# Performance work log

Hardware: AMD Instinct MI355X
Metric: run time of the kernel (lower is better)

The kernel has to match this reference:

```python
import jax, jax.numpy as jnp
import numpy as np

EPS = 0.5          # residual scaling (module __init__ eps)
N = 100_000        # num nodes
E = 1_250_000      # num edges (avg degree ~12.5)
D = 64             # feature dim


def setup_inputs() -> dict:
    key = jax.random.key(0)
    k1, k2, k3 = jax.random.split(key, 3)
    x = jax.random.normal(k1, (N, D), dtype=jnp.float32)
    src = jax.random.randint(k2, (E,), 0, N, dtype=jnp.int32)
    dst = jax.random.randint(k3, (E,), 0, N, dtype=jnp.int32)
    return {"x": x, "src": src, "dst": dst}


def reference(x, src, dst):
    n = x.shape[0]
    # out-degree of each node = number of edges with that node as source
    deg = jax.ops.segment_sum(jnp.ones(src.shape, dtype=x.dtype), src, num_segments=n)
    norm = jnp.power(jnp.maximum(deg, 1.0), -0.5)          # [N]
    edge_norm = norm[src] * norm[dst]                      # [E] (u_mul_v)
    msg = x[src] * edge_norm[:, None]                      # [E, D] (u_mul_e)
    h = jax.ops.segment_sum(msg, dst, num_segments=n)      # sum per destination
    return h + x * EPS
```

## Files before the change

### kernel.cpp

```cpp
#include <hip/hip_runtime.h>

constexpr int D        = 64;
constexpr float EPS    = 0.5f;
constexpr int BKT      = 256;
constexpr int CAPB_MAX = 4096;
constexpr int EPB      = 8192;
constexpr int PTHREADS = 512;
constexpr int EPT      = EPB / PTHREADS;
constexpr int GTHREADS = 1024;
constexpr int NBMAX    = 1024;
constexpr int MAXOVF   = 65536;

__device__ __forceinline__ unsigned int f2bf(float f) {
    unsigned int u = __float_as_uint(f);
    return (u + 0x7FFFu + ((u >> 16) & 1u)) >> 16;
}
__device__ __forceinline__ float bf2f_lo(unsigned int v) { return __uint_as_float(v << 16); }
__device__ __forceinline__ float bf2f_hi(unsigned int v) { return __uint_as_float(v & 0xFFFF0000u); }


__global__ __launch_bounds__(PTHREADS)
void partition_kernel(const int* __restrict__ src, const int* __restrict__ dst,
                      int* __restrict__ curD, int* __restrict__ curS,
                      unsigned int* __restrict__ rec, unsigned char* __restrict__ srec,
                      int* __restrict__ ovf_cnt, int* __restrict__ ovf,
                      int* __restrict__ sovf_cnt, int* __restrict__ sovf,
                      int E, int NB, int capb) {
    __shared__ int histD[NBMAX];
    __shared__ int histS[NBMAX];
    __shared__ int startD[NBMAX];
    __shared__ int startS[NBMAX];
    const int base = blockIdx.x * EPB;
    const int tid  = threadIdx.x;
    const bool full = (base + EPB) <= E;
    for (int b = tid; b < NB; b += PTHREADS) { histD[b] = 0; histS[b] = 0; }
    __syncthreads();

    if (full) {
        const int4* s4 = (const int4*)(src + base);
        const int4* d4 = (const int4*)(dst + base);
        #pragma unroll
        for (int k = 0; k < EPT / 4; ++k) {
            int4 sv = s4[tid + k * PTHREADS];
            int4 dv = d4[tid + k * PTHREADS];
            atomicAdd(&histD[dv.x >> 8], 1); atomicAdd(&histS[sv.x >> 8], 1);
            atomicAdd(&histD[dv.y >> 8], 1); atomicAdd(&histS[sv.y >> 8], 1);
            atomicAdd(&histD[dv.z >> 8], 1); atomicAdd(&histS[sv.z >> 8], 1);
            atomicAdd(&histD[dv.w >> 8], 1); atomicAdd(&histS[sv.w >> 8], 1);
        }
    } else {
        for (int k = 0; k < EPT; ++k) {
            int e = base + tid + k * PTHREADS;
            if (e < E) {
                atomicAdd(&histD[dst[e] >> 8], 1);
                atomicAdd(&histS[src[e] >> 8], 1);
            }
        }
    }
    __syncthreads();
    for (int b = tid; b < NB; b += PTHREADS) {
        int c = histD[b];
        startD[b] = (c > 0) ? atomicAdd(&curD[b], c) : 0;
        histD[b] = 0;
        int c2 = histS[b];
        startS[b] = (c2 > 0) ? atomicAdd(&curS[b], c2) : 0;
        histS[b] = 0;
    }
    __syncthreads();
    if (full) {
        const int4* s4 = (const int4*)(src + base);
        const int4* d4 = (const int4*)(dst + base);
        #pragma unroll
        for (int k = 0; k < EPT / 4; ++k) {
            int4 sv = s4[tid + k * PTHREADS];
            int4 dv = d4[tid + k * PTHREADS];
            int ss[4] = {sv.x, sv.y, sv.z, sv.w};
            int tt[4] = {dv.x, dv.y, dv.z, dv.w};
            #pragma unroll
            for (int j = 0; j < 4; ++j) {
                int s = ss[j], t = tt[j];
                int bD = t >> 8;
                int r  = atomicAdd(&histD[bD], 1);
                int p  = startD[bD] + r;
                if (p < capb) {
                    rec[(size_t)bD * capb + p] = ((unsigned int)s << 8) | (unsigned int)(t & (BKT - 1));
                } else {
                    int i = atomicAdd(ovf_cnt, 1);
                    if (i < MAXOVF) { ovf[2 * i] = s; ovf[2 * i + 1] = t; }
                }
                int bS = s >> 8;
                int r2 = atomicAdd(&histS[bS], 1);
                int p2 = startS[bS] + r2;
                if (p2 < capb) {
                    srec[(size_t)bS * capb + p2] = (unsigned char)(s & (BKT - 1));
                } else {
                    int i = atomicAdd(sovf_cnt, 1);
                    if (i < MAXOVF) sovf[i] = s;
                }
            }
        }
    } else {
        for (int k = 0; k < EPT; ++k) {
            int e = base + tid + k * PTHREADS;
            if (e < E) {
                int s = src[e], t = dst[e];
                int bD = t >> 8;
                int r  = atomicAdd(&histD[bD], 1);
                int p  = startD[bD] + r;
                if (p < capb) {
                    rec[(size_t)bD * capb + p] = ((unsigned int)s << 8) | (unsigned int)(t & (BKT - 1));
                } else {
                    int i = atomicAdd(ovf_cnt, 1);
                    if (i < MAXOVF) { ovf[2 * i] = s; ovf[2 * i + 1] = t; }
                }
                int bS = s >> 8;
                int r2 = atomicAdd(&histS[bS], 1);
                int p2 = startS[bS] + r2;
                if (p2 < capb) {
                    srec[(size_t)bS * capb + p2] = (unsigned char)(s & (BKT - 1));
                } else {
                    int i = atomicAdd(sovf_cnt, 1);
                    if (i < MAXOVF) sovf[i] = s;
                }
            }
        }
    }
}

__global__ __launch_bounds__(256)
void normyh_kernel(const unsigned char* __restrict__ srec, const int* __restrict__ curS,
                   const int* __restrict__ sovf_cnt, const int* __restrict__ sovf,
                   const float2* __restrict__ x2, unsigned int* __restrict__ yh,
                   float* __restrict__ norm, int n, int capb) {
    const int b   = blockIdx.x;
    const int tid = threadIdx.x;
    __shared__ int hist[BKT];
    __shared__ float nrm[BKT];
    hist[tid] = 0;
    __syncthreads();
    int cnt = curS[b];
    if (cnt > capb) cnt = capb;
    const unsigned int* s4 = (const unsigned int*)(srec + (size_t)b * capb);
    int nw = cnt >> 2;
    for (int i = tid; i < nw; i += 256) {
        unsigned int w = s4[i];
        atomicAdd(&hist[w & 255u], 1);
        atomicAdd(&hist[(w >> 8) & 255u], 1);
        atomicAdd(&hist[(w >> 16) & 255u], 1);
        atomicAdd(&hist[w >> 24], 1);
    }
    for (int i = (nw << 2) + tid; i < cnt; i += 256)
        atomicAdd(&hist[srec[(size_t)b * capb + i]], 1);
    int oc = *sovf_cnt;
    if (oc > 0) {
        if (oc > MAXOVF) oc = MAXOVF;
        for (int i = tid; i < oc; i += 256) {
            int s = sovf[i];
            if ((s >> 8) == b) atomicAdd(&hist[s & (BKT - 1)], 1);
        }
    }
    __syncthreads();
    int node = b * BKT + tid;
    float nm = rsqrtf(fmaxf((float)hist[tid], 1.0f));
    nrm[tid] = nm;
    if (node < n) norm[node] = nm;
    __syncthreads();
    int nodes = n - b * BKT;
    if (nodes > BKT) nodes = BKT;
    if (nodes < 0) nodes = 0;
    int total = nodes * (D / 2);
    size_t gbase = (size_t)b * BKT * (D / 2);
    for (int i = tid; i < total; i += 256) {
        float2 v = x2[gbase + i];
        float nm2 = nrm[i >> 5];
        yh[gbase + i] = f2bf(v.x * nm2) | (f2bf(v.y * nm2) << 16);
    }
}

__global__ __launch_bounds__(GTHREADS)
void sortgather_kernel(const unsigned int* __restrict__ rec, const int* __restrict__ curD,
                       const float* __restrict__ norm, const uint4* __restrict__ yr4,
                       const float4* __restrict__ x4, float4* __restrict__ out4,
                       int n, int capb) {
    __shared__ unsigned int recs[CAPB_MAX];
    __shared__ int srcs[CAPB_MAX];
    __shared__ int hist[BKT];
    __shared__ int rankb[BKT];
    __shared__ int rsL[BKT];
    __shared__ float nrmL[BKT];
    __shared__ int wsum[BKT / 64];
    const int b   = blockIdx.x;
    const int tid = threadIdx.x;

    int cnt = curD[b];
    if (cnt > capb) cnt = capb;
    for (int i = tid; i < cnt; i += GTHREADS) recs[i] = rec[(size_t)b * capb + i];
    if (tid < BKT) {
        hist[tid] = 0;
        int node = b * BKT + tid;
        nrmL[tid] = (node < n) ? norm[node] : 1.0f;
    }
    __syncthreads();
    for (int i = tid; i < cnt; i += GTHREADS) atomicAdd(&hist[recs[i] & (BKT - 1)], 1);
    __syncthreads();
    {
        const int lane = tid & 63;
        int v = (tid < BKT) ? hist[tid] : 0;
        #pragma unroll
        for (int off = 1; off < 64; off <<= 1) {
            int t = __shfl_up(v, off);
            if (lane >= off) v += t;
        }
        if (tid < BKT && lane == 63) wsum[tid >> 6] = v;
        __syncthreads();
        if (tid < BKT) {
            int w = tid >> 6, add = 0;
            #pragma unroll
            for (int i = 0; i < BKT / 64; ++i)
                if (i < w) add += wsum[i];
            int excl = v + add - hist[tid];
            rankb[tid] = excl;
            rsL[tid]   = excl;
        }
    }
    __syncthreads();
    for (int i = tid; i < cnt; i += GTHREADS) {
        unsigned int v = recs[i];
        int pos = atomicAdd(&rankb[v & (BKT - 1)], 1);
        srcs[pos] = (int)(v >> 8);
    }
    __syncthreads();

    const int wave = tid >> 6;
    const int lane = tid & 63;
    const int fl   = lane & 7;
    const int oct  = lane >> 3;
    #pragma unroll
    for (int r = 0; r < BKT / 128; ++r) {
        int ln   = r * 128 + wave * 8 + oct;
        int node = b * BKT + ln;
        bool valid = node < n;
        int rsl = valid ? rsL[ln]  : 0;
        int cl  = valid ? hist[ln] : 0;
        int m = cl;
        m = max(m, __shfl_xor(m, 8));
        m = max(m, __shfl_xor(m, 16));
        m = max(m, __shfl_xor(m, 32));
        float a0 = 0.f, a1 = 0.f, a2 = 0.f, a3 = 0.f;
        float a4 = 0.f, a5 = 0.f, a6 = 0.f, a7 = 0.f;
        for (int k = 0; k < m; k += 8) {
            int sb[8];
            #pragma unroll
            for (int j = 0; j < 8; ++j) {
                int kj = k + j;
                sb[j] = (kj < cl) ? srcs[rsl + kj] : -1;
            }
            #pragma unroll
            for (int j = 0; j < 8; ++j) {
                bool take = sb[j] >= 0;
                int s = take ? sb[j] : 0;
                uint4 v = yr4[(size_t)s * 8 + fl];
                if (!take) { v.x = 0u; v.y = 0u; v.z = 0u; v.w = 0u; }
                a0 += bf2f_lo(v.x); a1 += bf2f_hi(v.x);
                a2 += bf2f_lo(v.y); a3 += bf2f_hi(v.y);
                a4 += bf2f_lo(v.z); a5 += bf2f_hi(v.z);
                a6 += bf2f_lo(v.w); a7 += bf2f_hi(v.w);
            }
        }
        if (valid) {
            float nt = nrmL[ln];
            size_t basei = (size_t)node * 16 + fl * 2;
            float4 xv0 = x4[basei], xv1 = x4[basei + 1];
            float4 r0, r1;
            r0.x = a0 * nt + EPS * xv0.x;  r0.y = a1 * nt + EPS * xv0.y;
            r0.z = a2 * nt + EPS * xv0.z;  r0.w = a3 * nt + EPS * xv0.w;
            r1.x = a4 * nt + EPS * xv1.x;  r1.y = a5 * nt + EPS * xv1.y;
            r1.z = a6 * nt + EPS * xv1.z;  r1.w = a7 * nt + EPS * xv1.w;
            out4[basei] = r0;
            out4[basei + 1] = r1;
        }
    }
}

__global__ void cleanup_kernel(const float* __restrict__ x, const float* __restrict__ norm,
                               const int* __restrict__ ovf_cnt, const int* __restrict__ ovf,
                               float* __restrict__ out) {
    int cnt = *ovf_cnt;
    if (cnt > MAXOVF) cnt = MAXOVF;
    long long total = (long long)cnt * D;
    long long stride = (long long)gridDim.x * blockDim.x;
    for (long long i = blockIdx.x * (long long)blockDim.x + threadIdx.x; i < total; i += stride) {
        int e = (int)(i >> 6), d = (int)(i & 63);
        int s = ovf[2 * e], t = ovf[2 * e + 1];
        atomicAdd(&out[(size_t)t * D + d], norm[s] * norm[t] * x[(size_t)s * D + d]);
    }
}


__global__ void fb_hist(const int* __restrict__ src, int* __restrict__ deg, int E) {
    int e = blockIdx.x * blockDim.x + threadIdx.x;
    if (e < E) atomicAdd(&deg[src[e]], 1);
}
__global__ void fb_norm(const int* __restrict__ deg, float* __restrict__ norm, int n) {
    int i = blockIdx.x * blockDim.x + threadIdx.x;
    if (i < n) norm[i] = rsqrtf(fmaxf((float)deg[i], 1.0f));
}
__global__ void fb_init_out(const float4* __restrict__ x, float4* __restrict__ out, int n4) {
    int i = blockIdx.x * blockDim.x + threadIdx.x;
    if (i < n4) {
        float4 v = x[i];
        out[i] = make_float4(v.x * EPS, v.y * EPS, v.z * EPS, v.w * EPS);
    }
}
__global__ void fb_scatter(const float* __restrict__ x, const int* __restrict__ src,
                           const int* __restrict__ dst, const float* __restrict__ norm,
                           float* __restrict__ out, int E) {
    long long tid = (long long)blockIdx.x * blockDim.x + threadIdx.x;
    int e = (int)(tid >> 6), d = (int)(tid & 63);
    if (e < E) {
        int s = src[e], t = dst[e];
        atomicAdd(&out[(size_t)t * D + d], norm[s] * norm[t] * x[(size_t)s * D + d]);
    }
}


extern "C" void kernel_launch(void* const* d_in, const int* in_sizes, int n_in,
                              void* d_out, int out_size, void* d_ws, size_t ws_size,
                              hipStream_t stream) {
    const float* x   = (const float*)d_in[0];
    const int*   src = (const int*)d_in[1];
    const int*   dst = (const int*)d_in[2];
    float* out = (float*)d_out;

    const int ND = in_sizes[0];
    const int E  = in_sizes[1];
    const int n  = ND / D;
    const int NB = (n + BKT - 1) / BKT;
    constexpr int B = 256;
    const int NB64 = (NB + 63) & ~63;

    int capb = 0;
    for (int c : {4096, 3584}) {
        size_t srecB = ((size_t)NB * c + 15) & ~15ull;
        size_t need = (size_t)NB * c * 4
                    + srecB
                    + (size_t)ND * 2
                    + (size_t)n * 4
                    + (size_t)(2 * NB64 + 128) * 4
                    + (size_t)3 * MAXOVF * 4;
        if (need <= ws_size) { capb = c; break; }
    }

    if (NB <= NBMAX && capb > 0 && n < (1 << 24)) {
        unsigned int* rec   = (unsigned int*)d_ws;
        unsigned char* srec = (unsigned char*)(rec + (size_t)NB * capb);
        size_t srecB        = ((size_t)NB * capb + 15) & ~15ull;
        unsigned int* yh    = (unsigned int*)(srec + srecB);
        float* norm         = (float*)(yh + ND / 2);
        int* curD           = (int*)(norm + n);
        int* curS           = curD + NB64;
        int* ovf_cnt        = curS + NB64;
        int* sovf_cnt       = ovf_cnt + 64;
        int* ovf            = sovf_cnt + 64;
        int* sovf           = ovf + 2 * MAXOVF;

        hipMemsetAsync(curD, 0, (size_t)(2 * NB64 + 128) * 4, stream);
        partition_kernel<<<(E + EPB - 1) / EPB, PTHREADS, 0, stream>>>(src, dst, curD, curS,
                                                                       rec, srec, ovf_cnt, ovf,
                                                                       sovf_cnt, sovf, E, NB, capb);
        normyh_kernel<<<NB, B, 0, stream>>>(srec, curS, sovf_cnt, sovf,
                                            (const float2*)x, yh, norm, n, capb);
        sortgather_kernel<<<NB, GTHREADS, 0, stream>>>(rec, curD, norm, (const uint4*)yh,
                                                       (const float4*)x, (float4*)out, n, capb);
        cleanup_kernel<<<32, B, 0, stream>>>(x, norm, ovf_cnt, ovf, out);
    } else {
        int*   deg  = (int*)d_ws;
        float* norm = (float*)d_ws + n;
        hipMemsetAsync(deg, 0, (size_t)n * sizeof(int), stream);
        fb_hist<<<(E + B - 1) / B, B, 0, stream>>>(src, deg, E);
        fb_norm<<<(n + B - 1) / B, B, 0, stream>>>(deg, norm, n);
        fb_init_out<<<(ND / 4 + B - 1) / B, B, 0, stream>>>((const float4*)x, (float4*)out, ND / 4);
        long long total = (long long)E * D;
        fb_scatter<<<(int)((total + B - 1) / B), B, 0, stream>>>(x, src, dst, norm, out, E);
    }
}
```

Measured before the change: 140.7 us.

## Replace global atomic bucketing with per-block local sort and offset tables

The partition kernel now counting-sorts its edge chunk in shared memory and writes the sorted chunk contiguously. It also records per-block bucket offset tables, replacing global atomic cursors, fixed-capacity buckets, overflow lists, the memset and the cleanup kernel. The norm and gather kernels rebuild each bucket by scanning the offset tables and pulling the small per-block segments. The gather kernel processes oversized buckets in chunks. This removes global atomics and scattered global writes, but adds many short, poorly coalesced segment reads and strided table reads downstream.

```diff
diff --git a/kernel.cpp b/kernel.cpp
--- a/kernel.cpp
+++ b/kernel.cpp
@@ -3,13 +3,13 @@
 constexpr int D        = 64;
 constexpr float EPS    = 0.5f;
 constexpr int BKT      = 256;
-constexpr int CAPB_MAX = 4096;
-constexpr int EPB      = 8192;
+constexpr int CAPB     = 6144;
+constexpr int EPB      = 4096;
 constexpr int PTHREADS = 512;
 constexpr int EPT      = EPB / PTHREADS;
 constexpr int GTHREADS = 1024;
 constexpr int NBMAX    = 1024;
-constexpr int MAXOVF   = 65536;
+constexpr int MAXBLK   = 1024;
 
 __device__ __forceinline__ unsigned int f2bf(float f) {
     unsigned int u = __float_as_uint(f);
@@ -21,18 +21,26 @@
 
 __global__ __launch_bounds__(PTHREADS)
 void partition_kernel(const int* __restrict__ src, const int* __restrict__ dst,
-                      int* __restrict__ curD, int* __restrict__ curS,
-                      unsigned int* __restrict__ rec, unsigned char* __restrict__ srec,
-                      int* __restrict__ ovf_cnt, int* __restrict__ ovf,
-                      int* __restrict__ sovf_cnt, int* __restrict__ sovf,
-                      int E, int NB, int capb) {
+                      unsigned int* __restrict__ recB, unsigned char* __restrict__ srecB,
+                      unsigned short* __restrict__ tabD, unsigned short* __restrict__ tabS,
+                      int E, int NB, int NBP) {
+    __shared__ unsigned int  srt[EPB];
+    __shared__ unsigned char ssrt[EPB];
     __shared__ int histD[NBMAX];
     __shared__ int histS[NBMAX];
-    __shared__ int startD[NBMAX];
-    __shared__ int startS[NBMAX];
-    const int base = blockIdx.x * EPB;
+    __shared__ unsigned int rsD[NBMAX];
+    __shared__ unsigned int rsS[NBMAX];
+    __shared__ unsigned int wsums[PTHREADS / 64];
+    __shared__ unsigned int carry;
+
+    const int blk  = blockIdx.x;
+    const int base = blk * EPB;
     const int tid  = threadIdx.x;
-    const bool full = (base + EPB) <= E;
+    const int lane = tid & 63;
+    const int wid  = tid >> 6;
+    const int cnt  = min(EPB, E - base);
+    const bool full = (cnt == EPB);
+
     for (int b = tid; b < NB; b += PTHREADS) { histD[b] = 0; histS[b] = 0; }
     __syncthreads();
 
@@ -50,23 +58,73 @@
         }
     } else {
         for (int k = 0; k < EPT; ++k) {
-            int e = base + tid + k * PTHREADS;
-            if (e < E) {
-                atomicAdd(&histD[dst[e] >> 8], 1);
-                atomicAdd(&histS[src[e] >> 8], 1);
-            }
-        }
-    }
-    __syncthreads();
-    for (int b = tid; b < NB; b += PTHREADS) {
-        int c = histD[b];
-        startD[b] = (c > 0) ? atomicAdd(&curD[b], c) : 0;
-        histD[b] = 0;
-        int c2 = histS[b];
-        startS[b] = (c2 > 0) ? atomicAdd(&curS[b], c2) : 0;
-        histS[b] = 0;
-    }
-    __syncthreads();
+            int e = tid + k * PTHREADS;
+            if (e < cnt) {
+                atomicAdd(&histD[dst[base + e] >> 8], 1);
+                atomicAdd(&histS[src[base + e] >> 8], 1);
+            }
+        }
+    }
+    __syncthreads();
+
+    if (tid == 0) carry = 0;
+    __syncthreads();
+    for (int bp = 0; bp < NB; bp += PTHREADS) {
+        int idx = bp + tid;
+        unsigned int orig = (idx < NB) ? (unsigned int)histD[idx] : 0u;
+        if (idx < NB) histD[idx] = 0;
+        unsigned int v = orig;
+        #pragma unroll
+        for (int off = 1; off < 64; off <<= 1) {
+            unsigned int t = __shfl_up(v, off);
+            if (lane >= off) v += t;
+        }
+        if (lane == 63) wsums[wid] = v;
+        __syncthreads();
+        unsigned int add = carry;
+        for (int w = 0; w < wid; ++w) add += wsums[w];
+        if (idx < NB) rsD[idx] = v - orig + add;
+        __syncthreads();
+        if (tid == 0) {
+            unsigned int s = carry;
+            for (int w = 0; w < PTHREADS / 64; ++w) s += wsums[w];
+            carry = s;
+        }
+        __syncthreads();
+    }
+    if (tid == 0) carry = 0;
+    __syncthreads();
+    for (int bp = 0; bp < NB; bp += PTHREADS) {
+        int idx = bp + tid;
+        unsigned int orig = (idx < NB) ? (unsigned int)histS[idx] : 0u;
+        if (idx < NB) histS[idx] = 0;
+        unsigned int v = orig;
+        #pragma unroll
+        for (int off = 1; off < 64; off <<= 1) {
+            unsigned int t = __shfl_up(v, off);
+            if (lane >= off) v += t;
+        }
+        if (lane == 63) wsums[wid] = v;
+        __syncthreads();
+        unsigned int add = carry;
+        for (int w = 0; w < wid; ++w) add += wsums[w];
+        if (idx < NB) rsS[idx] = v - orig + add;
+        __syncthreads();
+        if (tid == 0) {
+            unsigned int s = carry;
+            for (int w = 0; w < PTHREADS / 64; ++w) s += wsums[w];
+            carry = s;
+        }
+        __syncthreads();
+    }
+
+    for (int b = tid; b <= NB; b += PTHREADS) {
+        unsigned short vD = (unsigned short)((b < NB) ? rsD[b] : (unsigned int)cnt);
+        unsigned short vS = (unsigned short)((b < NB) ? rsS[b] : (unsigned int)cnt);
+        tabD[(size_t)blk * NBP + b] = vD;
+        tabS[(size_t)blk * NBP + b] = vS;
+    }
+
     if (full) {
         const int4* s4 = (const int4*)(src + base);
         const int4* d4 = (const int4*)(dst + base);
@@ -81,83 +139,53 @@
                 int s = ss[j], t = tt[j];
                 int bD = t >> 8;
                 int r  = atomicAdd(&histD[bD], 1);
-                int p  = startD[bD] + r;
-                if (p < capb) {
-                    rec[(size_t)bD * capb + p] = ((unsigned int)s << 8) | (unsigned int)(t & (BKT - 1));
-                } else {
-                    int i = atomicAdd(ovf_cnt, 1);
-                    if (i < MAXOVF) { ovf[2 * i] = s; ovf[2 * i + 1] = t; }
-                }
+                srt[rsD[bD] + r] = ((unsigned int)s << 8) | (unsigned int)(t & (BKT - 1));
                 int bS = s >> 8;
                 int r2 = atomicAdd(&histS[bS], 1);
-                int p2 = startS[bS] + r2;
-                if (p2 < capb) {
-                    srec[(size_t)bS * capb + p2] = (unsigned char)(s & (BKT - 1));
-                } else {
-                    int i = atomicAdd(sovf_cnt, 1);
-                    if (i < MAXOVF) sovf[i] = s;
-                }
+                ssrt[rsS[bS] + r2] = (unsigned char)(s & (BKT - 1));
             }
         }
     } else {
         for (int k = 0; k < EPT; ++k) {
-            int e = base + tid + k * PTHREADS;
-            if (e < E) {
-                int s = src[e], t = dst[e];
+            int e = tid + k * PTHREADS;
+            if (e < cnt) {
+                int s = src[base + e], t = dst[base + e];
                 int bD = t >> 8;
                 int r  = atomicAdd(&histD[bD], 1);
-                int p  = startD[bD] + r;
-                if (p < capb) {
-                    rec[(size_t)bD * capb + p] = ((unsigned int)s << 8) | (unsigned int)(t & (BKT - 1));
-                } else {
-                    int i = atomicAdd(ovf_cnt, 1);
-                    if (i < MAXOVF) { ovf[2 * i] = s; ovf[2 * i + 1] = t; }
-                }
+                srt[rsD[bD] + r] = ((unsigned int)s << 8) | (unsigned int)(t & (BKT - 1));
                 int bS = s >> 8;
                 int r2 = atomicAdd(&histS[bS], 1);
-                int p2 = startS[bS] + r2;
-                if (p2 < capb) {
-                    srec[(size_t)bS * capb + p2] = (unsigned char)(s & (BKT - 1));
-                } else {
-                    int i = atomicAdd(sovf_cnt, 1);
-                    if (i < MAXOVF) sovf[i] = s;
-                }
-            }
-        }
+                ssrt[rsS[bS] + r2] = (unsigned char)(s & (BKT - 1));
+            }
+        }
+    }
+    __syncthreads();
+
+    {
+        uint4* go = (uint4*)(recB + (size_t)blk * EPB);
+        const uint4* gi = (const uint4*)srt;
+        for (int i = tid; i < EPB / 4; i += PTHREADS) go[i] = gi[i];
+        uint4* so = (uint4*)(srecB + (size_t)blk * EPB);
+        const uint4* si = (const uint4*)ssrt;
+        for (int i = tid; i < EPB / 16; i += PTHREADS) so[i] = si[i];
     }
 }
 
 __global__ __launch_bounds__(256)
-void normyh_kernel(const unsigned char* __restrict__ srec, const int* __restrict__ curS,
-                   const int* __restrict__ sovf_cnt, const int* __restrict__ sovf,
+void normyh_kernel(const unsigned char* __restrict__ srecB, const unsigned short* __restrict__ tabS,
                    const float2* __restrict__ x2, unsigned int* __restrict__ yh,
-                   float* __restrict__ norm, int n, int capb) {
+                   float* __restrict__ norm, int n, int NBLK, int NBP) {
     const int b   = blockIdx.x;
     const int tid = threadIdx.x;
     __shared__ int hist[BKT];
     __shared__ float nrm[BKT];
     hist[tid] = 0;
     __syncthreads();
-    int cnt = curS[b];
-    if (cnt > capb) cnt = capb;
-    const unsigned int* s4 = (const unsigned int*)(srec + (size_t)b * capb);
-    int nw = cnt >> 2;
-    for (int i = tid; i < nw; i += 256) {
-        unsigned int w = s4[i];
-        atomicAdd(&hist[w & 255u], 1);
-        atomicAdd(&hist[(w >> 8) & 255u], 1);
-        atomicAdd(&hist[(w >> 16) & 255u], 1);
-        atomicAdd(&hist[w >> 24], 1);
-    }
-    for (int i = (nw << 2) + tid; i < cnt; i += 256)
-        atomicAdd(&hist[srec[(size_t)b * capb + i]], 1);
-    int oc = *sovf_cnt;
-    if (oc > 0) {
-        if (oc > MAXOVF) oc = MAXOVF;
-        for (int i = tid; i < oc; i += 256) {
-            int s = sovf[i];
-            if ((s >> 8) == b) atomicAdd(&hist[s & (BKT - 1)], 1);
-        }
+    for (int blk = tid; blk < NBLK; blk += 256) {
+        int o0 = tabS[(size_t)blk * NBP + b];
+        int o1 = tabS[(size_t)blk * NBP + b + 1];
+        const unsigned char* p = srecB + (size_t)blk * EPB;
+        for (int j = o0; j < o1; ++j) atomicAdd(&hist[p[j]], 1);
     }
     __syncthreads();
     int node = b * BKT + tid;
@@ -178,121 +206,163 @@
 }
 
 __global__ __launch_bounds__(GTHREADS)
-void sortgather_kernel(const unsigned int* __restrict__ rec, const int* __restrict__ curD,
+void sortgather_kernel(const unsigned int* __restrict__ recB, const unsigned short* __restrict__ tabD,
                        const float* __restrict__ norm, const uint4* __restrict__ yr4,
                        const float4* __restrict__ x4, float4* __restrict__ out4,
-                       int n, int capb) {
-    __shared__ unsigned int recs[CAPB_MAX];
-    __shared__ int srcs[CAPB_MAX];
+                       int n, int NBLK, int NBP) {
+    __shared__ unsigned int recs[CAPB];
+    __shared__ unsigned int srcs[CAPB];
+    __shared__ unsigned short segoff[MAXBLK];
+    __shared__ unsigned int dstoff[MAXBLK + 1];
     __shared__ int hist[BKT];
     __shared__ int rankb[BKT];
     __shared__ int rsL[BKT];
     __shared__ float nrmL[BKT];
-    __shared__ int wsum[BKT / 64];
-    const int b   = blockIdx.x;
-    const int tid = threadIdx.x;
-
-    int cnt = curD[b];
-    if (cnt > capb) cnt = capb;
-    for (int i = tid; i < cnt; i += GTHREADS) recs[i] = rec[(size_t)b * capb + i];
+    __shared__ unsigned int wsums[GTHREADS / 64];
+    __shared__ unsigned int carry;
+    const int b    = blockIdx.x;
+    const int tid  = threadIdx.x;
+    const int lane = tid & 63;
+    const int wid  = tid >> 6;
+
+    for (int blk = tid; blk < NBLK; blk += GTHREADS) {
+        unsigned int o0 = tabD[(size_t)blk * NBP + b];
+        unsigned int o1 = tabD[(size_t)blk * NBP + b + 1];
+        segoff[blk] = (unsigned short)o0;
+        dstoff[blk] = o1 - o0;
+    }
     if (tid < BKT) {
-        hist[tid] = 0;
         int node = b * BKT + tid;
         nrmL[tid] = (node < n) ? norm[node] : 1.0f;
     }
-    __syncthreads();
-    for (int i = tid; i < cnt; i += GTHREADS) atomicAdd(&hist[recs[i] & (BKT - 1)], 1);
-    __syncthreads();
-    {
-        const int lane = tid & 63;
-        int v = (tid < BKT) ? hist[tid] : 0;
+    if (tid == 0) carry = 0;
+    __syncthreads();
+    for (int bp = 0; bp < NBLK; bp += GTHREADS) {
+        int idx = bp + tid;
+        unsigned int orig = (idx < NBLK) ? dstoff[idx] : 0u;
+        unsigned int v = orig;
         #pragma unroll
         for (int off = 1; off < 64; off <<= 1) {
-            int t = __shfl_up(v, off);
+            unsigned int t = __shfl_up(v, off);
             if (lane >= off) v += t;
         }
-        if (tid < BKT && lane == 63) wsum[tid >> 6] = v;
-        __syncthreads();
-        if (tid < BKT) {
-            int w = tid >> 6, add = 0;
+        if (lane == 63) wsums[wid] = v;
+        __syncthreads();
+        unsigned int add = carry;
+        for (int w = 0; w < wid; ++w) add += wsums[w];
+        if (idx < NBLK) dstoff[idx] = v - orig + add;
+        __syncthreads();
+        if (tid == 0) {
+            unsigned int s = carry;
+            for (int w = 0; w < GTHREADS / 64; ++w) s += wsums[w];
+            carry = s;
+        }
+        __syncthreads();
+    }
+    if (tid == 0) dstoff[NBLK] = carry;
+    __syncthreads();
+    const int cnt = (int)dstoff[NBLK];
+    const int nch = (cnt > CAPB) ? (cnt + CAPB - 1) / CAPB : 1;
+
+    const int fl  = lane & 7;
+    const int oct = lane >> 3;
+
+    for (int c = 0; c < nch; ++c) {
+        const unsigned int lo = (unsigned int)c * CAPB;
+        const unsigned int hi = min((unsigned int)cnt, lo + (unsigned int)CAPB);
+        const int wlen = (int)(hi - lo);
+        for (int blk = wid; blk < NBLK; blk += GTHREADS / 64) {
+            unsigned int dbase = dstoff[blk], dend = dstoff[blk + 1];
+            unsigned int s0 = max(dbase, lo), s1 = min(dend, hi);
+            if (s0 < s1) {
+                size_t glo = (size_t)blk * EPB + segoff[blk] + (s0 - dbase);
+                for (unsigned int j = lane; j < s1 - s0; j += 64)
+                    recs[s0 - lo + j] = recB[glo + j];
+            }
+        }
+        __syncthreads();
+        if (tid < BKT) hist[tid] = 0;
+        __syncthreads();
+        for (int i = tid; i < wlen; i += GTHREADS) atomicAdd(&hist[recs[i] & (BKT - 1)], 1);
+        __syncthreads();
+        {
+            int v = (tid < BKT) ? hist[tid] : 0;
             #pragma unroll
-            for (int i = 0; i < BKT / 64; ++i)
-                if (i < w) add += wsum[i];
-            int excl = v + add - hist[tid];
-            rankb[tid] = excl;
-            rsL[tid]   = excl;
-        }
-    }
-    __syncthreads();
-    for (int i = tid; i < cnt; i += GTHREADS) {
-        unsigned int v = recs[i];
-        int pos = atomicAdd(&rankb[v & (BKT - 1)], 1);
-        srcs[pos] = (int)(v >> 8);
-    }
-    __syncthreads();
-
-    const int wave = tid >> 6;
-    const int lane = tid & 63;
-    const int fl   = lane & 7;
-    const int oct  = lane >> 3;
-    #pragma unroll
-    for (int r = 0; r < BKT / 128; ++r) {
-        int ln   = r * 128 + wave * 8 + oct;
-        int node = b * BKT + ln;
-        bool valid = node < n;
-        int rsl = valid ? rsL[ln]  : 0;
-        int cl  = valid ? hist[ln] : 0;
-        int m = cl;
-        m = max(m, __shfl_xor(m, 8));
-        m = max(m, __shfl_xor(m, 16));
-        m = max(m, __shfl_xor(m, 32));
-        float a0 = 0.f, a1 = 0.f, a2 = 0.f, a3 = 0.f;
-        float a4 = 0.f, a5 = 0.f, a6 = 0.f, a7 = 0.f;
-        for (int k = 0; k < m; k += 8) {
-            int sb[8];
-            #pragma unroll
-            for (int j = 0; j < 8; ++j) {
-                int kj = k + j;
-                sb[j] = (kj < cl) ? srcs[rsl + kj] : -1;
-            }
-            #pragma unroll
-            for (int j = 0; j < 8; ++j) {
-                bool take = sb[j] >= 0;
-                int s = take ? sb[j] : 0;
-                uint4 v = yr4[(size_t)s * 8 + fl];
-                if (!take) { v.x = 0u; v.y = 0u; v.z = 0u; v.w = 0u; }
-                a0 += bf2f_lo(v.x); a1 += bf2f_hi(v.x);
-                a2 += bf2f_lo(v.y); a3 += bf2f_hi(v.y);
-                a4 += bf2f_lo(v.z); a5 += bf2f_hi(v.z);
-                a6 += bf2f_lo(v.w); a7 += bf2f_hi(v.w);
-            }
-        }
-        if (valid) {
-            float nt = nrmL[ln];
-            size_t basei = (size_t)node * 16 + fl * 2;
-            float4 xv0 = x4[basei], xv1 = x4[basei + 1];
-            float4 r0, r1;
-            r0.x = a0 * nt + EPS * xv0.x;  r0.y = a1 * nt + EPS * xv0.y;
-            r0.z = a2 * nt + EPS * xv0.z;  r0.w = a3 * nt + EPS * xv0.w;
-            r1.x = a4 * nt + EPS * xv1.x;  r1.y = a5 * nt + EPS * xv1.y;
-            r1.z = a6 * nt + EPS * xv1.z;  r1.w = a7 * nt + EPS * xv1.w;
-            out4[basei] = r0;
-            out4[basei + 1] = r1;
-        }
-    }
-}
-
-__global__ void cleanup_kernel(const float* __restrict__ x, const float* __restrict__ norm,
-                               const int* __restrict__ ovf_cnt, const int* __restrict__ ovf,
-                               float* __restrict__ out) {
-    int cnt = *ovf_cnt;
-    if (cnt > MAXOVF) cnt = MAXOVF;
-    long long total = (long long)cnt * D;
-    long long stride = (long long)gridDim.x * blockDim.x;
-    for (long long i = blockIdx.x * (long long)blockDim.x + threadIdx.x; i < total; i += stride) {
-        int e = (int)(i >> 6), d = (int)(i & 63);
-        int s = ovf[2 * e], t = ovf[2 * e + 1];
-        atomicAdd(&out[(size_t)t * D + d], norm[s] * norm[t] * x[(size_t)s * D + d]);
+            for (int off = 1; off < 64; off <<= 1) {
+                int t = __shfl_up(v, off);
+                if (lane >= off) v += t;
+            }
+            if (tid < BKT && lane == 63) wsums[wid] = (unsigned int)v;
+            __syncthreads();
+            if (tid < BKT) {
+                int add = 0;
+                for (int w = 0; w < wid; ++w) add += (int)wsums[w];
+                int excl = v + add - hist[tid];
+                rankb[tid] = excl;
+                rsL[tid]   = excl;
+            }
+        }
+        __syncthreads();
+        for (int i = tid; i < wlen; i += GTHREADS) {
+            unsigned int v = recs[i];
+            int pos = atomicAdd(&rankb[v & (BKT - 1)], 1);
+            srcs[pos] = (int)(v >> 8);
+        }
+        __syncthreads();
+
+        #pragma unroll
+        for (int r = 0; r < BKT / 128; ++r) {
+            int ln   = r * 128 + wid * 8 + oct;
+            int node = b * BKT + ln;
+            bool valid = node < n;
+            int rsl = valid ? rsL[ln]  : 0;
+            int cl  = valid ? hist[ln] : 0;
+            int m = cl;
+            m = max(m, __shfl_xor(m, 8));
+            m = max(m, __shfl_xor(m, 16));
+            m = max(m, __shfl_xor(m, 32));
+            float a0 = 0.f, a1 = 0.f, a2 = 0.f, a3 = 0.f;
+            float a4 = 0.f, a5 = 0.f, a6 = 0.f, a7 = 0.f;
+            for (int k = 0; k < m; k += 8) {
+                int sb[8];
+                #pragma unroll
+                for (int j = 0; j < 8; ++j) {
+                    int kj = k + j;
+                    sb[j] = (kj < cl) ? (int)srcs[rsl + kj] : -1;
+                }
+                #pragma unroll
+                for (int j = 0; j < 8; ++j) {
+                    bool take = sb[j] >= 0;
+                    int s = take ? sb[j] : 0;
+                    uint4 v = yr4[(size_t)s * 8 + fl];
+                    if (!take) { v.x = 0u; v.y = 0u; v.z = 0u; v.w = 0u; }
+                    a0 += bf2f_lo(v.x); a1 += bf2f_hi(v.x);
+                    a2 += bf2f_lo(v.y); a3 += bf2f_hi(v.y);
+                    a4 += bf2f_lo(v.z); a5 += bf2f_hi(v.z);
+                    a6 += bf2f_lo(v.w); a7 += bf2f_hi(v.w);
+                }
+            }
+            if (valid) {
+                float nt = nrmL[ln];
+                size_t basei = (size_t)node * 16 + fl * 2;
+                float4 r0, r1;
+                if (c == 0) {
+                    float4 xv0 = x4[basei], xv1 = x4[basei + 1];
+                    r0.x = a0 * nt + EPS * xv0.x;  r0.y = a1 * nt + EPS * xv0.y;
+                    r0.z = a2 * nt + EPS * xv0.z;  r0.w = a3 * nt + EPS * xv0.w;
+                    r1.x = a4 * nt + EPS * xv1.x;  r1.y = a5 * nt + EPS * xv1.y;
+                    r1.z = a6 * nt + EPS * xv1.z;  r1.w = a7 * nt + EPS * xv1.w;
+                } else {
+                    float4 p0 = out4[basei], p1 = out4[basei + 1];
+                    r0.x = p0.x + a0 * nt;  r0.y = p0.y + a1 * nt;
+                    r0.z = p0.z + a2 * nt;  r0.w = p0.w + a3 * nt;
+                    r1.x = p1.x + a4 * nt;  r1.y = p1.y + a5 * nt;
+                    r1.z = p1.z + a6 * nt;  r1.w = p1.w + a7 * nt;
+                }
+                out4[basei] = r0;
+                out4[basei + 1] = r1;
+            }
+        }
     }
 }
 
@@ -335,44 +405,37 @@
     const int ND = in_sizes[0];
     const int E  = in_sizes[1];
     const int n  = ND / D;
-    const int NB = (n + BKT - 1) / BKT;
+    const int NB   = (n + BKT - 1) / BKT;
+    const int NBLK = (E + EPB - 1) / EPB;
+    const int NBP  = NB + 1;
     constexpr int B = 256;
-    const int NB64 = (NB + 63) & ~63;
-
-    int capb = 0;
-    for (int c : {4096, 3584}) {
-        size_t srecB = ((size_t)NB * c + 15) & ~15ull;
-        size_t need = (size_t)NB * c * 4
-                    + srecB
-                    + (size_t)ND * 2
-                    + (size_t)n * 4
-                    + (size_t)(2 * NB64 + 128) * 4
-                    + (size_t)3 * MAXOVF * 4;
-        if (need <= ws_size) { capb = c; break; }
-    }
-
-    if (NB <= NBMAX && capb > 0 && n < (1 << 24)) {
-        unsigned int* rec   = (unsigned int*)d_ws;
-        unsigned char* srec = (unsigned char*)(rec + (size_t)NB * capb);
-        size_t srecB        = ((size_t)NB * capb + 15) & ~15ull;
-        unsigned int* yh    = (unsigned int*)(srec + srecB);
-        float* norm         = (float*)(yh + ND / 2);
-        int* curD           = (int*)(norm + n);
-        int* curS           = curD + NB64;
-        int* ovf_cnt        = curS + NB64;
-        int* sovf_cnt       = ovf_cnt + 64;
-        int* ovf            = sovf_cnt + 64;
-        int* sovf           = ovf + 2 * MAXOVF;
-
-        hipMemsetAsync(curD, 0, (size_t)(2 * NB64 + 128) * 4, stream);
-        partition_kernel<<<(E + EPB - 1) / EPB, PTHREADS, 0, stream>>>(src, dst, curD, curS,
-                                                                       rec, srec, ovf_cnt, ovf,
-                                                                       sovf_cnt, sovf, E, NB, capb);
-        normyh_kernel<<<NB, B, 0, stream>>>(srec, curS, sovf_cnt, sovf,
-                                            (const float2*)x, yh, norm, n, capb);
-        sortgather_kernel<<<NB, GTHREADS, 0, stream>>>(rec, curD, norm, (const uint4*)yh,
-                                                       (const float4*)x, (float4*)out, n, capb);
-        cleanup_kernel<<<32, B, 0, stream>>>(x, norm, ovf_cnt, ovf, out);
+
+    size_t off = 0;
+    auto take = [&](size_t bytes) { size_t o = off; off = (off + bytes + 15) & ~15ull; return o; };
+    size_t o_rec  = take((size_t)NBLK * EPB * 4);
+    size_t o_srec = take((size_t)NBLK * EPB);
+    size_t o_tabD = take((size_t)NBLK * NBP * 2);
+    size_t o_tabS = take((size_t)NBLK * NBP * 2);
+    size_t o_yh   = take((size_t)ND * 2);
+    size_t o_norm = take((size_t)n * 4);
+    size_t need = off;
+
+    if (NB <= NBMAX && NBLK <= MAXBLK && n < (1 << 24) && need <= ws_size && E > 0) {
+        char* ws = (char*)d_ws;
+        unsigned int*   recB  = (unsigned int*)(ws + o_rec);
+        unsigned char*  srecB = (unsigned char*)(ws + o_srec);
+        unsigned short* tabD  = (unsigned short*)(ws + o_tabD);
+        unsigned short* tabS  = (unsigned short*)(ws + o_tabS);
+        unsigned int*   yh    = (unsigned int*)(ws + o_yh);
+        float*          norm  = (float*)(ws + o_norm);
+
+        partition_kernel<<<NBLK, PTHREADS, 0, stream>>>(src, dst, recB, srecB,
+                                                        tabD, tabS, E, NB, NBP);
+        normyh_kernel<<<NB, B, 0, stream>>>(srecB, tabS, (const float2*)x, yh, norm,
+                                            n, NBLK, NBP);
+        sortgather_kernel<<<NB, GTHREADS, 0, stream>>>(recB, tabD, norm, (const uint4*)yh,
+                                                       (const float4*)x, (float4*)out,
+                                                       n, NBLK, NBP);
     } else {
         int*   deg  = (int*)d_ws;
         float* norm = (float*)d_ws + n;
```

Measured after the change: 179.6 us. 27.7% more time.
